# Performance work log

Hardware: AMD Instinct MI355X
Metric: run time of the kernel (lower is better)

Reference implementation:

```python
import jax, jax.numpy as jnp
import numpy as np

NUM_USER = 262144
NUM_ITEM = 262144
DIM = 64
NNZ = 1_250_000
N_LAYERS = 3


def setup_inputs() -> dict:
    key = jax.random.key(0)
    ku, ki, kr, kc, kv = jax.random.split(key, 5)
    n = NUM_USER + NUM_ITEM
    # xavier_uniform bound for (rows, cols) weight
    a = float(np.sqrt(6.0 / (NUM_USER + DIM)))
    user_emb = jax.random.uniform(ku, (NUM_USER, DIM), minval=-a, maxval=a, dtype=jnp.float32)
    b = float(np.sqrt(6.0 / (NUM_ITEM + DIM)))
    item_emb = jax.random.uniform(ki, (NUM_ITEM, DIM), minval=-b, maxval=b, dtype=jnp.float32)
    adj_rows = jax.random.randint(kr, (NNZ,), 0, n, dtype=jnp.int32)
    adj_cols = jax.random.randint(kc, (NNZ,), 0, n, dtype=jnp.int32)
    # normalized adjacency values are small positive floats
    adj_vals = jax.random.uniform(kv, (NNZ,), minval=0.0, maxval=0.1, dtype=jnp.float32)
    return {"user_emb": user_emb, "item_emb": item_emb,
            "adj_rows": adj_rows, "adj_cols": adj_cols, "adj_vals": adj_vals}


def reference(user_emb, item_emb, adj_rows, adj_cols, adj_vals):
    num_user = user_emb.shape[0]
    ego = jnp.concatenate([user_emb, item_emb], axis=0)  # [N, D]
    n = ego.shape[0]

    def spmm(x):
        # sparse.mm(adj, x): gather source rows, scale, scatter-add to dest rows
        msgs = adj_vals[:, None] * x[adj_cols]            # [NNZ, D]
        return jax.ops.segment_sum(msgs, adj_rows, num_segments=n)

    # running sum instead of stack+mean (same math: mean over L+1 layer outputs)
    acc = ego
    cur = ego
    for _ in range(N_LAYERS):
        cur = spmm(cur)
        acc = acc + cur
    mean_emb = acc / jnp.asarray(N_LAYERS + 1, dtype=ego.dtype)
    return mean_emb[:num_user], mean_emb[num_user:]
```

## Files before the change

kernel.cpp:

```cpp
#include <hip/hip_runtime.h>


constexpr int NUM_USER = 262144;
constexpr int NUM_ITEM = 262144;
constexpr int DIM      = 64;
constexpr int N_NODES  = NUM_USER + NUM_ITEM;
constexpr int NNZ      = 1250000;

constexpr int NBUCK = 256;
constexpr int ROWS_PER_BUCK = N_NODES / NBUCK;
constexpr int PB_BLOCKS = 512;
constexpr int CHUNK = (NNZ + PB_BLOCKS - 1) / PB_BLOCKS;
constexpr int BCAP = 6144;

__device__ __forceinline__ unsigned bfpack2(float a, float b) {
    unsigned ua = __float_as_uint(a); ua += 0x7fffu + ((ua >> 16) & 1u);
    unsigned ub = __float_as_uint(b); ub += 0x7fffu + ((ub >> 16) & 1u);
    return (ua >> 16) | (ub & 0xffff0000u);
}
__device__ __forceinline__ uint4 bfpack8(float4 a, float4 b) {
    return make_uint4(bfpack2(a.x, a.y), bfpack2(a.z, a.w),
                      bfpack2(b.x, b.y), bfpack2(b.z, b.w));
}
__device__ __forceinline__ void bfunpack8(uint4 u, float4& l, float4& h) {
    l.x = __uint_as_float(u.x << 16);
    l.y = __uint_as_float(u.x & 0xffff0000u);
    l.z = __uint_as_float(u.y << 16);
    l.w = __uint_as_float(u.y & 0xffff0000u);
    h.x = __uint_as_float(u.z << 16);
    h.y = __uint_as_float(u.z & 0xffff0000u);
    h.z = __uint_as_float(u.w << 16);
    h.w = __uint_as_float(u.w & 0xffff0000u);
}
__device__ __forceinline__ void fma4(float4& s, float v, const float4 x) {
    s.x = fmaf(v, x.x, s.x);
    s.y = fmaf(v, x.y, s.y);
    s.z = fmaf(v, x.z, s.z);
    s.w = fmaf(v, x.w, s.w);
}
__device__ __forceinline__ float4 add4(float4 a, float4 b) {
    return make_float4(a.x + b.x, a.y + b.y, a.z + b.z, a.w + b.w);
}

__global__ void bucket_count(const int* __restrict__ rows, int* __restrict__ bcnt) {
    __shared__ int lcnt[NBUCK];
    const int t = threadIdx.x;
    lcnt[t] = 0;
    __syncthreads();
    const int beg = blockIdx.x * CHUNK;
    const int end = min(beg + CHUNK, NNZ);
    for (int i = beg + t; i < end; i += 256)
        atomicAdd(&lcnt[rows[i] >> 11], 1);
    __syncthreads();
    bcnt[t * PB_BLOCKS + blockIdx.x] = lcnt[t];
}

__global__ void scan_bcnt(int* __restrict__ bcnt, int* __restrict__ tot) {
    __shared__ int tmp[256];
    const int b = blockIdx.x, t = threadIdx.x;
    const int a0 = bcnt[b * PB_BLOCKS + 2 * t];
    const int a1 = bcnt[b * PB_BLOCKS + 2 * t + 1];
    const int run = a0 + a1;
    tmp[t] = run;
    __syncthreads();
    for (int off = 1; off < 256; off <<= 1) {
        int x = (t >= off) ? tmp[t - off] : 0;
        __syncthreads();
        tmp[t] += x;
        __syncthreads();
    }
    const int excl = tmp[t] - run;
    bcnt[b * PB_BLOCKS + 2 * t]     = excl;
    bcnt[b * PB_BLOCKS + 2 * t + 1] = excl + a0;
    if (t == 255) tot[b] = tmp[255];
}

__global__ void scan_btot(const int* __restrict__ tot, int* __restrict__ bbase) {
    __shared__ int tmp[256];
    const int t = threadIdx.x;
    const int v = tot[t];
    tmp[t] = v;
    __syncthreads();
    for (int off = 1; off < 256; off <<= 1) {
        int x = (t >= off) ? tmp[t - off] : 0;
        __syncthreads();
        tmp[t] += x;
        __syncthreads();
    }
    bbase[t] = tmp[t] - v;
    if (t == 0) bbase[NBUCK] = NNZ;
}

__global__ void bucket_scatter(const int* __restrict__ rows, const int* __restrict__ cols,
                               const float* __restrict__ vals,
                               const int* __restrict__ bcnt, const int* __restrict__ bbase,
                               int2* __restrict__ eb, unsigned short* __restrict__ ebrow) {
    __shared__ int lbase[NBUCK];
    __shared__ int lofs[NBUCK];
    const int t = threadIdx.x;
    lbase[t] = bbase[t] + bcnt[t * PB_BLOCKS + blockIdx.x];
    lofs[t] = 0;
    __syncthreads();
    const int beg = blockIdx.x * CHUNK;
    const int end = min(beg + CHUNK, NNZ);
    for (int i = beg + t; i < end; i += 256) {
        const int r = rows[i];
        const int b = r >> 11;
        const int p = lbase[b] + atomicAdd(&lofs[b], 1);
        eb[p]    = make_int2(cols[i], __float_as_int(vals[i]));
        ebrow[p] = (unsigned short)(r & (ROWS_PER_BUCK - 1));
    }
}

__global__ void bucket_finalize(const int* __restrict__ bbase,
                                const int2* __restrict__ eb,
                                const unsigned short* __restrict__ ebrow,
                                int* __restrict__ row_ptr, int2* __restrict__ sc) {
    __shared__ int  lcnt[ROWS_PER_BUCK];
    __shared__ int  tmp[256];
    __shared__ int2 lout[BCAP];
    const int b    = blockIdx.x;
    const int t    = threadIdx.x;
    const int base = bbase[b];
    const int cnt  = bbase[b + 1] - base;
    for (int r = t; r < ROWS_PER_BUCK; r += 256) lcnt[r] = 0;
    __syncthreads();
    for (int i = t; i < cnt; i += 256)
        atomicAdd(&lcnt[ebrow[base + i]], 1);
    __syncthreads();
    int loc[8];
    int run = 0;
    #pragma unroll
    for (int k = 0; k < 8; ++k) { const int v = lcnt[t * 8 + k]; loc[k] = run; run += v; }
    tmp[t] = run;
    __syncthreads();
    for (int off = 1; off < 256; off <<= 1) {
        int x = (t >= off) ? tmp[t - off] : 0;
        __syncthreads();
        tmp[t] += x;
        __syncthreads();
    }
    const int excl = tmp[t] - run;
    #pragma unroll
    for (int k = 0; k < 8; ++k) lcnt[t * 8 + k] = loc[k] + excl;
    __syncthreads();
    for (int r = t; r < ROWS_PER_BUCK; r += 256)
        row_ptr[b * ROWS_PER_BUCK + r] = base + lcnt[r];
    if (b == NBUCK - 1 && t == 0) row_ptr[N_NODES] = NNZ;
    __syncthreads();
    if (cnt <= BCAP) {
        for (int i = t; i < cnt; i += 256) {
            const int p = atomicAdd(&lcnt[ebrow[base + i]], 1);
            lout[p] = eb[base + i];
        }
        __syncthreads();
        for (int i = t; i < cnt; i += 256)
            sc[base + i] = lout[i];
    } else {
        for (int i = t; i < cnt; i += 256) {
            const int p = atomicAdd(&lcnt[ebrow[base + i]], 1);
            sc[base + p] = eb[base + i];
        }
    }
}

__global__ void spmm_first(const int* __restrict__ ptr, const int2* __restrict__ sc,
                           const float4* __restrict__ ue4, const float4* __restrict__ ie4,
                           uint4* __restrict__ e1b) {
    const int row = blockIdx.x * 32 + (threadIdx.x >> 3);
    const int d8  = threadIdx.x & 7;
    const int beg = ptr[row];
    const int end = ptr[row + 1];
    float4 a0 = {0.f,0.f,0.f,0.f}, b0 = {0.f,0.f,0.f,0.f};
    float4 a1 = {0.f,0.f,0.f,0.f}, b1 = {0.f,0.f,0.f,0.f};
    int e = beg;
    for (; e + 2 <= end; e += 2) {
        const int2 A = sc[e];
        const int2 B = sc[e + 1];
        const float4* pa = (A.x < NUM_USER) ? ue4 + (size_t)A.x * 16
                                            : ie4 + (size_t)(A.x - NUM_USER) * 16;
        const float4* pb = (B.x < NUM_USER) ? ue4 + (size_t)B.x * 16
                                            : ie4 + (size_t)(B.x - NUM_USER) * 16;
        const float4 al = pa[2 * d8], ah = pa[2 * d8 + 1];
        const float4 bl = pb[2 * d8], bh = pb[2 * d8 + 1];
        const float va = __int_as_float(A.y);
        const float vb = __int_as_float(B.y);
        fma4(a0, va, al); fma4(b0, va, ah);
        fma4(a1, vb, bl); fma4(b1, vb, bh);
    }
    if (e < end) {
        const int2 A = sc[e];
        const float4* pa = (A.x < NUM_USER) ? ue4 + (size_t)A.x * 16
                                            : ie4 + (size_t)(A.x - NUM_USER) * 16;
        const float va = __int_as_float(A.y);
        fma4(a0, va, pa[2 * d8]); fma4(b0, va, pa[2 * d8 + 1]);
    }
    e1b[row * 8 + d8] = bfpack8(add4(a0, a1), add4(b0, b1));
}

__global__ void spmm_b2b(const int* __restrict__ ptr, const int2* __restrict__ sc,
                         const uint4* __restrict__ xb, uint4* __restrict__ yb) {
    const int row = blockIdx.x * 32 + (threadIdx.x >> 3);
    const int d8  = threadIdx.x & 7;
    const int beg = ptr[row];
    const int end = ptr[row + 1];
    float4 a0 = {0.f,0.f,0.f,0.f}, b0 = {0.f,0.f,0.f,0.f};
    float4 a1 = {0.f,0.f,0.f,0.f}, b1 = {0.f,0.f,0.f,0.f};
    int e = beg;
    for (; e + 2 <= end; e += 2) {
        const int2 A = sc[e];
        const int2 B = sc[e + 1];
        const uint4 xa = xb[A.x * 8 + d8];
        const uint4 xc = xb[B.x * 8 + d8];
        float4 l, h;
        bfunpack8(xa, l, h);
        fma4(a0, __int_as_float(A.y), l); fma4(b0, __int_as_float(A.y), h);
        bfunpack8(xc, l, h);
        fma4(a1, __int_as_float(B.y), l); fma4(b1, __int_as_float(B.y), h);
    }
    if (e < end) {
        const int2 A = sc[e];
        float4 l, h;
        bfunpack8(xb[A.x * 8 + d8], l, h);
        fma4(a0, __int_as_float(A.y), l); fma4(b0, __int_as_float(A.y), h);
    }
    yb[row * 8 + d8] = bfpack8(add4(a0, a1), add4(b0, b1));
}

__global__ void spmm_last(const int* __restrict__ ptr, const int2* __restrict__ sc,
                          const float4* __restrict__ ue4, const float4* __restrict__ ie4,
                          const uint4* __restrict__ e1b, const uint4* __restrict__ e2b,
                          float4* __restrict__ out4) {
    const int row = blockIdx.x * 32 + (threadIdx.x >> 3);
    const int d8  = threadIdx.x & 7;
    const int beg = ptr[row];
    const int end = ptr[row + 1];
    const int o8 = row * 8 + d8;
    const float4* pg = (row < NUM_USER) ? ue4 + (size_t)row * 16
                                        : ie4 + (size_t)(row - NUM_USER) * 16;
    const float4 gl = pg[2 * d8];
    const float4 gh = pg[2 * d8 + 1];
    const uint4 u1 = e1b[o8];
    const uint4 u2 = e2b[o8];
    float4 a0 = {0.f,0.f,0.f,0.f}, b0 = {0.f,0.f,0.f,0.f};
    float4 a1 = {0.f,0.f,0.f,0.f}, b1 = {0.f,0.f,0.f,0.f};
    int e = beg;
    for (; e + 2 <= end; e += 2) {
        const int2 A = sc[e];
        const int2 B = sc[e + 1];
        const uint4 xa = e2b[A.x * 8 + d8];
        const uint4 xc = e2b[B.x * 8 + d8];
        float4 l, h;
        bfunpack8(xa, l, h);
        fma4(a0, __int_as_float(A.y), l); fma4(b0, __int_as_float(A.y), h);
        bfunpack8(xc, l, h);
        fma4(a1, __int_as_float(B.y), l); fma4(b1, __int_as_float(B.y), h);
    }
    if (e < end) {
        const int2 A = sc[e];
        float4 l, h;
        bfunpack8(e2b[A.x * 8 + d8], l, h);
        fma4(a0, __int_as_float(A.y), l); fma4(b0, __int_as_float(A.y), h);
    }
    a0 = add4(a0, a1); b0 = add4(b0, b1);
    float4 l1, h1, l2, h2;
    bfunpack8(u1, l1, h1);
    bfunpack8(u2, l2, h2);
    float4 r0, r1;
    r0.x = (gl.x + l1.x + l2.x + a0.x) * 0.25f;
    r0.y = (gl.y + l1.y + l2.y + a0.y) * 0.25f;
    r0.z = (gl.z + l1.z + l2.z + a0.z) * 0.25f;
    r0.w = (gl.w + l1.w + l2.w + a0.w) * 0.25f;
    r1.x = (gh.x + h1.x + h2.x + b0.x) * 0.25f;
    r1.y = (gh.y + h1.y + h2.y + b0.y) * 0.25f;
    r1.z = (gh.z + h1.z + h2.z + b0.z) * 0.25f;
    r1.w = (gh.w + h1.w + h2.w + b0.w) * 0.25f;
    out4[row * 16 + 2 * d8]     = r0;
    out4[row * 16 + 2 * d8 + 1] = r1;
}

__global__ void lgcn_init(const float4* __restrict__ ue, const float4* __restrict__ ie,
                          float4* __restrict__ cur, float4* __restrict__ acc) {
    const long total  = (long)N_NODES * (DIM / 4);
    const long utotal = (long)NUM_USER * (DIM / 4);
    long i = (long)blockIdx.x * blockDim.x + threadIdx.x;
    const long stride = (long)gridDim.x * blockDim.x;
    for (; i < total; i += stride) {
        float4 v = (i < utotal) ? ue[i] : ie[i - utotal];
        cur[i] = v;
        acc[i] = v;
    }
}

__global__ void lgcn_spmm_atomic(const int* __restrict__ rows, const int* __restrict__ cols,
                                 const float* __restrict__ vals, const float* __restrict__ x,
                                 float* __restrict__ y) {
    const long total  = (long)NNZ * DIM;
    long t = (long)blockIdx.x * blockDim.x + threadIdx.x;
    const long stride = (long)gridDim.x * blockDim.x;
    for (; t < total; t += stride) {
        const int e = (int)(t >> 6);
        const int d = (int)(t & 63);
        atomicAdd(&y[((long)rows[e] << 6) + d], vals[e] * x[((long)cols[e] << 6) + d]);
    }
}

__global__ void lgcn_add(float4* __restrict__ acc, const float4* __restrict__ nxt, float scale) {
    const long total  = (long)N_NODES * (DIM / 4);
    long i = (long)blockIdx.x * blockDim.x + threadIdx.x;
    const long stride = (long)gridDim.x * blockDim.x;
    for (; i < total; i += stride) {
        float4 a = acc[i];
        const float4 b = nxt[i];
        a.x = (a.x + b.x) * scale;
        a.y = (a.y + b.y) * scale;
        a.z = (a.z + b.z) * scale;
        a.w = (a.w + b.w) * scale;
        acc[i] = a;
    }
}

extern "C" void kernel_launch(void* const* d_in, const int* in_sizes, int n_in,
                              void* d_out, int out_size, void* d_ws, size_t ws_size,
                              hipStream_t stream) {
    const float* ue   = (const float*)d_in[0];
    const float* ie   = (const float*)d_in[1];
    const int*   rows = (const int*)d_in[2];
    const int*   cols = (const int*)d_in[3];
    const float* vals = (const float*)d_in[4];
    float* out = (float*)d_out;

    const size_t embBytes  = (size_t)N_NODES * DIM * sizeof(float);
    const size_t embBytesH = embBytes / 2;
    char* ws = (char*)d_ws;
    uint4* e1b = (uint4*)ws;
    uint4* e2b = (uint4*)(ws + embBytesH);
    char* p = ws + 2 * embBytesH;
    int2* sc = (int2*)p;                 p += (size_t)NNZ * 8;
    int2* eb = (int2*)p;                 p += (size_t)NNZ * 8;
    unsigned short* ebrow = (unsigned short*)p; p += (size_t)NNZ * 2;
    int* row_ptr = (int*)p;              p += (size_t)(N_NODES + 1) * 4;
    int* bcnt    = (int*)p;              p += (size_t)NBUCK * PB_BLOCKS * 4;
    int* tot     = (int*)p;              p += (size_t)NBUCK * 4;
    int* bbase   = (int*)p;              p += (size_t)(NBUCK + 1) * 4;
    const size_t need = (size_t)(p - ws);

    if (ws_size >= need) {
        bucket_count   <<<PB_BLOCKS, 256, 0, stream>>>(rows, bcnt);
        scan_bcnt      <<<NBUCK,     256, 0, stream>>>(bcnt, tot);
        scan_btot      <<<1,         256, 0, stream>>>(tot, bbase);
        bucket_scatter <<<PB_BLOCKS, 256, 0, stream>>>(rows, cols, vals, bcnt, bbase,
                                                       eb, ebrow);
        bucket_finalize<<<NBUCK,     256, 0, stream>>>(bbase, eb, ebrow, row_ptr, sc);

        spmm_first<<<N_NODES / 32, 256, 0, stream>>>(row_ptr, sc,
                                                     (const float4*)ue, (const float4*)ie,
                                                     e1b);
        spmm_b2b  <<<N_NODES / 32, 256, 0, stream>>>(row_ptr, sc, e1b, e2b);
        spmm_last <<<N_NODES / 32, 256, 0, stream>>>(row_ptr, sc,
                                                     (const float4*)ue, (const float4*)ie,
                                                     e1b, e2b, (float4*)out);
    } else {
        float* buf0 = (float*)ws;
        float* buf1 = (float*)(ws + embBytes);
        lgcn_init<<<4096, 256, 0, stream>>>((const float4*)ue, (const float4*)ie,
                                            (float4*)buf0, (float4*)out);
        float* cur = buf0;
        float* nxt = buf1;
        for (int l = 0; l < 3; ++l) {
            hipMemsetAsync(nxt, 0, embBytes, stream);
            lgcn_spmm_atomic<<<2048, 256, 0, stream>>>(rows, cols, vals, cur, nxt);
            const float scale = (l == 2) ? 0.25f : 1.0f;
            lgcn_add<<<4096, 256, 0, stream>>>((float4*)out, (const float4*)nxt, scale);
            float* t = cur; cur = nxt; nxt = t;
        }
    }
}
```

Measured before the change: 263.0 us.

## Precompute ego+e1 partial sum, software-pipeline gathers, halve bucket-count blocks

After: 282.3 us. 1.07x slower.

```diff
diff --git a/kernel.cpp b/kernel.cpp
--- a/kernel.cpp
+++ b/kernel.cpp
@@ -9,7 +9,7 @@
 
 constexpr int NBUCK = 256;
 constexpr int ROWS_PER_BUCK = N_NODES / NBUCK;
-constexpr int PB_BLOCKS = 512;
+constexpr int PB_BLOCKS = 256;
 constexpr int CHUNK = (NNZ + PB_BLOCKS - 1) / PB_BLOCKS;
 constexpr int BCAP = 6144;
 
@@ -58,10 +58,8 @@
 __global__ void scan_bcnt(int* __restrict__ bcnt, int* __restrict__ tot) {
     __shared__ int tmp[256];
     const int b = blockIdx.x, t = threadIdx.x;
-    const int a0 = bcnt[b * PB_BLOCKS + 2 * t];
-    const int a1 = bcnt[b * PB_BLOCKS + 2 * t + 1];
-    const int run = a0 + a1;
-    tmp[t] = run;
+    const int v = bcnt[b * PB_BLOCKS + t];
+    tmp[t] = v;
     __syncthreads();
     for (int off = 1; off < 256; off <<= 1) {
         int x = (t >= off) ? tmp[t - off] : 0;
@@ -69,9 +67,7 @@
         tmp[t] += x;
         __syncthreads();
     }
-    const int excl = tmp[t] - run;
-    bcnt[b * PB_BLOCKS + 2 * t]     = excl;
-    bcnt[b * PB_BLOCKS + 2 * t + 1] = excl + a0;
+    bcnt[b * PB_BLOCKS + t] = tmp[t] - v;
     if (t == 255) tot[b] = tmp[255];
 }
 
@@ -166,11 +162,15 @@
 
 __global__ void spmm_first(const int* __restrict__ ptr, const int2* __restrict__ sc,
                            const float4* __restrict__ ue4, const float4* __restrict__ ie4,
-                           uint4* __restrict__ e1b) {
+                           uint4* __restrict__ e1b, uint4* __restrict__ s1b) {
     const int row = blockIdx.x * 32 + (threadIdx.x >> 3);
     const int d8  = threadIdx.x & 7;
     const int beg = ptr[row];
     const int end = ptr[row + 1];
+    const float4* pg = (row < NUM_USER) ? ue4 + (size_t)row * 16
+                                        : ie4 + (size_t)(row - NUM_USER) * 16;
+    const float4 gl = pg[2 * d8];
+    const float4 gh = pg[2 * d8 + 1];
     float4 a0 = {0.f,0.f,0.f,0.f}, b0 = {0.f,0.f,0.f,0.f};
     float4 a1 = {0.f,0.f,0.f,0.f}, b1 = {0.f,0.f,0.f,0.f};
     int e = beg;
@@ -195,7 +195,10 @@
         const float va = __int_as_float(A.y);
         fma4(a0, va, pa[2 * d8]); fma4(b0, va, pa[2 * d8 + 1]);
     }
-    e1b[row * 8 + d8] = bfpack8(add4(a0, a1), add4(b0, b1));
+    const float4 sl = add4(a0, a1), sh = add4(b0, b1);
+    const int o8 = row * 8 + d8;
+    e1b[o8] = bfpack8(sl, sh);
+    s1b[o8] = bfpack8(add4(sl, gl), add4(sh, gh));
 }
 
 __global__ void spmm_b2b(const int* __restrict__ ptr, const int2* __restrict__ sc,
@@ -206,75 +209,84 @@
     const int end = ptr[row + 1];
     float4 a0 = {0.f,0.f,0.f,0.f}, b0 = {0.f,0.f,0.f,0.f};
     float4 a1 = {0.f,0.f,0.f,0.f}, b1 = {0.f,0.f,0.f,0.f};
-    int e = beg;
-    for (; e + 2 <= end; e += 2) {
-        const int2 A = sc[e];
-        const int2 B = sc[e + 1];
-        const uint4 xa = xb[A.x * 8 + d8];
-        const uint4 xc = xb[B.x * 8 + d8];
-        float4 l, h;
-        bfunpack8(xa, l, h);
-        fma4(a0, __int_as_float(A.y), l); fma4(b0, __int_as_float(A.y), h);
-        bfunpack8(xc, l, h);
-        fma4(a1, __int_as_float(B.y), l); fma4(b1, __int_as_float(B.y), h);
-    }
-    if (e < end) {
-        const int2 A = sc[e];
-        float4 l, h;
-        bfunpack8(xb[A.x * 8 + d8], l, h);
-        fma4(a0, __int_as_float(A.y), l); fma4(b0, __int_as_float(A.y), h);
+    bool h0 = beg < end, h1 = beg + 1 < end;
+    int2 A0 = {0, 0}, A1 = {0, 0};
+    uint4 X0 = {0,0,0,0}, X1 = {0,0,0,0};
+    if (h0) { A0 = sc[beg];     X0 = xb[A0.x * 8 + d8]; }
+    if (h1) { A1 = sc[beg + 1]; X1 = xb[A1.x * 8 + d8]; }
+    int e = beg + 2;
+    while (h0) {
+        const bool nh0 = e < end, nh1 = e + 1 < end;
+        int2 nA0 = {0, 0}, nA1 = {0, 0};
+        uint4 nX0 = {0,0,0,0}, nX1 = {0,0,0,0};
+        if (nh0) { nA0 = sc[e];     nX0 = xb[nA0.x * 8 + d8]; }
+        if (nh1) { nA1 = sc[e + 1]; nX1 = xb[nA1.x * 8 + d8]; }
+        {
+            float4 l, h;
+            bfunpack8(X0, l, h);
+            fma4(a0, __int_as_float(A0.y), l); fma4(b0, __int_as_float(A0.y), h);
+        }
+        if (h1) {
+            float4 l, h;
+            bfunpack8(X1, l, h);
+            fma4(a1, __int_as_float(A1.y), l); fma4(b1, __int_as_float(A1.y), h);
+        }
+        h0 = nh0; h1 = nh1; A0 = nA0; A1 = nA1; X0 = nX0; X1 = nX1;
+        e += 2;
     }
     yb[row * 8 + d8] = bfpack8(add4(a0, a1), add4(b0, b1));
 }
 
 __global__ void spmm_last(const int* __restrict__ ptr, const int2* __restrict__ sc,
-                          const float4* __restrict__ ue4, const float4* __restrict__ ie4,
-                          const uint4* __restrict__ e1b, const uint4* __restrict__ e2b,
+                          const uint4* __restrict__ s1b, const uint4* __restrict__ e2b,
                           float4* __restrict__ out4) {
     const int row = blockIdx.x * 32 + (threadIdx.x >> 3);
     const int d8  = threadIdx.x & 7;
     const int beg = ptr[row];
     const int end = ptr[row + 1];
     const int o8 = row * 8 + d8;
-    const float4* pg = (row < NUM_USER) ? ue4 + (size_t)row * 16
-                                        : ie4 + (size_t)(row - NUM_USER) * 16;
-    const float4 gl = pg[2 * d8];
-    const float4 gh = pg[2 * d8 + 1];
-    const uint4 u1 = e1b[o8];
+    const uint4 u1 = s1b[o8];
     const uint4 u2 = e2b[o8];
     float4 a0 = {0.f,0.f,0.f,0.f}, b0 = {0.f,0.f,0.f,0.f};
     float4 a1 = {0.f,0.f,0.f,0.f}, b1 = {0.f,0.f,0.f,0.f};
-    int e = beg;
-    for (; e + 2 <= end; e += 2) {
-        const int2 A = sc[e];
-        const int2 B = sc[e + 1];
-        const uint4 xa = e2b[A.x * 8 + d8];
-        const uint4 xc = e2b[B.x * 8 + d8];
-        float4 l, h;
-        bfunpack8(xa, l, h);
-        fma4(a0, __int_as_float(A.y), l); fma4(b0, __int_as_float(A.y), h);
-        bfunpack8(xc, l, h);
-        fma4(a1, __int_as_float(B.y), l); fma4(b1, __int_as_float(B.y), h);
-    }
-    if (e < end) {
-        const int2 A = sc[e];
-        float4 l, h;
-        bfunpack8(e2b[A.x * 8 + d8], l, h);
-        fma4(a0, __int_as_float(A.y), l); fma4(b0, __int_as_float(A.y), h);
+    bool h0 = beg < end, h1 = beg + 1 < end;
+    int2 A0 = {0, 0}, A1 = {0, 0};
+    uint4 X0 = {0,0,0,0}, X1 = {0,0,0,0};
+    if (h0) { A0 = sc[beg];     X0 = e2b[A0.x * 8 + d8]; }
+    if (h1) { A1 = sc[beg + 1]; X1 = e2b[A1.x * 8 + d8]; }
+    int e = beg + 2;
+    while (h0) {
+        const bool nh0 = e < end, nh1 = e + 1 < end;
+        int2 nA0 = {0, 0}, nA1 = {0, 0};
+        uint4 nX0 = {0,0,0,0}, nX1 = {0,0,0,0};
+        if (nh0) { nA0 = sc[e];     nX0 = e2b[nA0.x * 8 + d8]; }
+        if (nh1) { nA1 = sc[e + 1]; nX1 = e2b[nA1.x * 8 + d8]; }
+        {
+            float4 l, h;
+            bfunpack8(X0, l, h);
+            fma4(a0, __int_as_float(A0.y), l); fma4(b0, __int_as_float(A0.y), h);
+        }
+        if (h1) {
+            float4 l, h;
+            bfunpack8(X1, l, h);
+            fma4(a1, __int_as_float(A1.y), l); fma4(b1, __int_as_float(A1.y), h);
+        }
+        h0 = nh0; h1 = nh1; A0 = nA0; A1 = nA1; X0 = nX0; X1 = nX1;
+        e += 2;
     }
     a0 = add4(a0, a1); b0 = add4(b0, b1);
-    float4 l1, h1, l2, h2;
-    bfunpack8(u1, l1, h1);
+    float4 l1, h1f, l2, h2;
+    bfunpack8(u1, l1, h1f);
     bfunpack8(u2, l2, h2);
     float4 r0, r1;
-    r0.x = (gl.x + l1.x + l2.x + a0.x) * 0.25f;
-    r0.y = (gl.y + l1.y + l2.y + a0.y) * 0.25f;
-    r0.z = (gl.z + l1.z + l2.z + a0.z) * 0.25f;
-    r0.w = (gl.w + l1.w + l2.w + a0.w) * 0.25f;
-    r1.x = (gh.x + h1.x + h2.x + b0.x) * 0.25f;
-    r1.y = (gh.y + h1.y + h2.y + b0.y) * 0.25f;
-    r1.z = (gh.z + h1.z + h2.z + b0.z) * 0.25f;
-    r1.w = (gh.w + h1.w + h2.w + b0.w) * 0.25f;
+    r0.x = (l1.x + l2.x + a0.x) * 0.25f;
+    r0.y = (l1.y + l2.y + a0.y) * 0.25f;
+    r0.z = (l1.z + l2.z + a0.z) * 0.25f;
+    r0.w = (l1.w + l2.w + a0.w) * 0.25f;
+    r1.x = (h1f.x + h2.x + b0.x) * 0.25f;
+    r1.y = (h1f.y + h2.y + b0.y) * 0.25f;
+    r1.z = (h1f.z + h2.z + b0.z) * 0.25f;
+    r1.w = (h1f.w + h2.w + b0.w) * 0.25f;
     out4[row * 16 + 2 * d8]     = r0;
     out4[row * 16 + 2 * d8 + 1] = r1;
 }
@@ -335,7 +347,8 @@
     char* ws = (char*)d_ws;
     uint4* e1b = (uint4*)ws;
     uint4* e2b = (uint4*)(ws + embBytesH);
-    char* p = ws + 2 * embBytesH;
+    uint4* s1b = (uint4*)(ws + 2 * embBytesH);
+    char* p = ws + 3 * embBytesH;
     int2* sc = (int2*)p;                 p += (size_t)NNZ * 8;
     int2* eb = (int2*)p;                 p += (size_t)NNZ * 8;
     unsigned short* ebrow = (unsigned short*)p; p += (size_t)NNZ * 2;
@@ -355,11 +368,9 @@
 
         spmm_first<<<N_NODES / 32, 256, 0, stream>>>(row_ptr, sc,
                                                      (const float4*)ue, (const float4*)ie,
-                                                     e1b);
+                                                     e1b, s1b);
         spmm_b2b  <<<N_NODES / 32, 256, 0, stream>>>(row_ptr, sc, e1b, e2b);
-        spmm_last <<<N_NODES / 32, 256, 0, stream>>>(row_ptr, sc,
-                                                     (const float4*)ue, (const float4*)ie,
-                                                     e1b, e2b, (float4*)out);
+        spmm_last <<<N_NODES / 32, 256, 0, stream>>>(row_ptr, sc, s1b, e2b, (float4*)out);
     } else {
         float* buf0 = (float*)ws;
         float* buf1 = (float*)(ws + embBytes);
```
